# Kernel optimization log

Measured on AMD Instinct MI355X. Metric: run time of the kernel, lower is better.

Reference implementation:

```python
import jax, jax.numpy as jnp
import numpy as np

LOCAL_RANGE = 2
STRIDE = 2
NEG = 1e10

def stride_sparse_mask(N):
    i = np.arange(N)[:, None]
    j = np.arange(N)[None, :]
    d = np.abs(j - i)
    return ((d <= LOCAL_RANGE) | (d % STRIDE == 0)).astype(np.float32)

def setup_inputs() -> dict:
    key = jax.random.key(0)
    k1, k2, k3, k4 = jax.random.split(key, 4)
    B, S, D, H = 4, 2048, 512, 8
    # glorot-uniform-like scale for (D, D) weight slices
    lim = np.sqrt(6.0 / (D + D)).astype(np.float32)
    inputs = jax.random.normal(k1, (B, 1, S, D), dtype=jnp.float32)
    Wq = jax.random.uniform(k2, (H, D, D), minval=-lim, maxval=lim, dtype=jnp.float32)
    Wk = jax.random.uniform(k3, (H, D, D), minval=-lim, maxval=lim, dtype=jnp.float32)
    Wv = jax.random.uniform(k4, (H, D, D), minval=-lim, maxval=lim, dtype=jnp.float32)
    return {"inputs": inputs, "Wq": Wq, "Wk": Wk, "Wv": Wv}

def reference(inputs, Wq, Wk, Wv):
    # inputs: (B, 1, S, D); Wq/Wk/Wv: (H, D, D)
    B, _, S, D = inputs.shape
    H = Wq.shape[0]
    x = inputs[:, 0]  # (B, S, D)
    mask = jnp.asarray(stride_sparse_mask(S))  # (S, S), static
    # Batched over heads: equivalent to the original per-head Python loop.
    Q = jnp.einsum('bsd,hdk->bhsk', x, Wq)
    K = jnp.einsum('bsd,hdk->bhsk', x, Wk)
    V = jnp.einsum('bsd,hdk->bhsk', x, Wv)
    scores = jnp.einsum('bhsk,bhtk->bhst', Q, K) / jnp.sqrt(jnp.float32(D))
    # Original applies the 0/1 mask once (head 0) or twice (later heads);
    # double application is mathematically identical to a single one.
    scores = scores * mask - NEG * (1.0 - mask)
    attn = jax.nn.softmax(scores, axis=-1)
    out = jnp.einsum('bhst,bhtk->bhsk', attn, V)  # (B, H, S, D)
    total = jnp.mean(out, axis=1)  # average over heads
    return total[:, None, :, :]  # (B, 1, S, D)
```

## Files before the change

### kernel.cpp

```cpp
#include <hip/hip_runtime.h>
#include <stdint.h>

#define Bdim 4
#define Sdim 2048
#define Ddim 512
#define Hdim 8
#define Mdim (Bdim*Sdim)
#define Shalf 1024

typedef __attribute__((ext_vector_type(8))) short bf16x8;
typedef __attribute__((ext_vector_type(4))) float f32x4;
typedef __attribute__((ext_vector_type(4))) int i32x4;

#define SCALE 0.044194173824159216f
#define LOG2E 1.4426950408889634f

__device__ __forceinline__ unsigned short f2bf(float f){
  union { float f; unsigned int u; } v; v.f = f;
  unsigned int u = v.u + 0x7FFFu + ((v.u >> 16) & 1u);
  return (unsigned short)(u >> 16);
}

__device__ __forceinline__ void gl_lds16(const void* g, void* l){
  __builtin_amdgcn_global_load_lds(
      (const __attribute__((address_space(1))) unsigned int*)g,
      (__attribute__((address_space(3))) unsigned int*)l, 16, 0, 0);
}

__device__ __forceinline__ int permrow(int m){
  return (m & ~2047) | ((m & 1) << 10) | ((m & 2047) >> 1);
}

__global__ void cvt_x(const float* __restrict__ x, unsigned short* __restrict__ xb, int n8){
  int i = blockIdx.x*blockDim.x + threadIdx.x;
  if (i >= n8) return;
  const float4* p = (const float4*)x + (size_t)i*2;
  float4 a = p[0], b = p[1];
  union { unsigned short s[8]; i32x4 v; } o;
  o.s[0]=f2bf(a.x); o.s[1]=f2bf(a.y); o.s[2]=f2bf(a.z); o.s[3]=f2bf(a.w);
  o.s[4]=f2bf(b.x); o.s[5]=f2bf(b.y); o.s[6]=f2bf(b.z); o.s[7]=f2bf(b.w);
  ((i32x4*)xb)[i] = o.v;
}

__global__ void twk(const float* __restrict__ Wq, const float* __restrict__ Wk,
                    const float* __restrict__ Wv, unsigned short* __restrict__ Wt){
  __shared__ float t[32][33];
  int z = blockIdx.z;
  const float* W = (z < Hdim ? Wq : (z < 2*Hdim ? Wk : Wv)) + (size_t)(z % Hdim)*Ddim*Ddim;
  int n0 = blockIdx.x*32, k0 = blockIdx.y*32;
  #pragma unroll
  for (int i=0;i<4;i++){
    int k = k0 + threadIdx.y + i*8;
    t[threadIdx.y + i*8][threadIdx.x] = W[(size_t)k*Ddim + n0 + threadIdx.x];
  }
  __syncthreads();
  #pragma unroll
  for (int i=0;i<4;i++){
    int n = threadIdx.y + i*8;
    Wt[(size_t)z*Ddim*Ddim + (size_t)(n0+n)*Ddim + k0 + threadIdx.x] = f2bf(t[threadIdx.x][n]);
  }
}

__launch_bounds__(256, 2)
__global__ void proj(const unsigned short* __restrict__ xb,
                     const unsigned short* __restrict__ Wt,
                     unsigned short* __restrict__ Qb,
                     unsigned short* __restrict__ Kb,
                     unsigned short* __restrict__ Vtb,
                     int h0, int g)
{
  __shared__ unsigned short smem[16640];
  int tid = threadIdx.x, w = tid>>6, lane = tid&63;
  int wm = w>>1, wn = w&1;
  int y = blockIdx.y, g4 = 4*g;
  int type = y / g4; int rem = y - type*g4;
  int hrel = rem >> 2, nt = rem & 3;
  int m0 = blockIdx.x * 128, n0 = nt * 128;
  int l15 = lane&15, l4 = lane>>4;

  const unsigned short* Bsrc = Wt + (size_t)(type*Hdim + h0 + hrel)*Ddim*Ddim;

  f32x4 acc[4][4];
  #pragma unroll
  for (int i=0;i<4;i++)
    #pragma unroll
    for (int j=0;j<4;j++){ f32x4 z={0.f,0.f,0.f,0.f}; acc[i][j]=z; }

  for (int kt=0; kt<16; ++kt){
    int k0 = kt*32;
    #pragma unroll
    for (int i=0;i<2;i++){
      int row = i*64 + w*16 + (lane>>2);
      int cb  = lane&3;
      gl_lds16(xb   + (size_t)(m0+row)*Ddim + k0 + cb*8, (char*)smem + i*4096 + w*1024);
      gl_lds16(Bsrc + (size_t)(n0+row)*Ddim + k0 + cb*8, (char*)smem + 8192 + i*4096 + w*1024);
    }
    __syncthreads();
    bf16x8 af[4], bfr[4];
    #pragma unroll
    for (int i=0;i<4;i++){
      af[i]  = *(const bf16x8*)&smem[(wm*64 + i*16 + l15)*32 + l4*8];
      bfr[i] = *(const bf16x8*)&smem[4096 + (wn*64 + i*16 + l15)*32 + l4*8];
    }
    #pragma unroll
    for (int i=0;i<4;i++)
      #pragma unroll
      for (int j=0;j<4;j++)
        acc[i][j] = __builtin_amdgcn_mfma_f32_16x16x32_bf16(af[i], bfr[j], acc[i][j], 0,0,0);
    __syncthreads();
  }

  if (type < 2){
    unsigned short* Ob = (type==0 ? Qb : Kb) + (size_t)hrel*Mdim*Ddim;
    #pragma unroll
    for (int i=0;i<4;i++){
      int mb = m0 + wm*64 + i*16 + (l4<<2);
      #pragma unroll
      for (int j=0;j<4;j++){
        int col = n0 + wn*64 + j*16 + l15;
        #pragma unroll
        for (int r=0;r<4;r++)
          Ob[(size_t)permrow(mb + r)*Ddim + col] = f2bf(acc[i][j][r]);
      }
    }
  } else {
    #pragma unroll
    for (int i=0;i<4;i++){
      int ml = wm*64 + i*16 + (l4<<2);
      #pragma unroll
      for (int j=0;j<4;j++){
        int nl = wn*64 + j*16 + l15;
        #pragma unroll
        for (int r=0;r<4;r++)
          smem[(ml + r)*130 + nl] = f2bf(acc[i][j][r]);
      }
    }
    __syncthreads();
    unsigned short* Ovt = Vtb + (size_t)hrel*Ddim*Mdim;
    int bb  = m0 >> 11;
    int ib0 = (m0 & 2047) >> 1;
    #pragma unroll
    for (int c=0;c<8;c++){
      int nl = c*16 + (tid>>4);
      int il = (tid&15)*4;
      #pragma unroll
      for (int pp=0; pp<2; pp++){
        union { unsigned short s[4]; uint2 v; } pk;
        #pragma unroll
        for (int ii=0;ii<4;ii++) pk.s[ii] = smem[(2*(il+ii)+pp)*130 + nl];
        *(uint2*)&Ovt[(size_t)(n0+nl)*Mdim + bb*Sdim + pp*Shalf + ib0 + il] = pk.v;
      }
    }
  }
}

__device__ __forceinline__ void stage_dense(const unsigned short* Kbase, int krow0,
                                            const unsigned short* Vblk, int vcol0,
                                            char* KsB, char* VsB, int w, int lane)
{
  int l15 = lane&15, l4 = lane>>4;
  #pragma unroll
  for (int jj=0;jj<4;jj++){
    int bi = w*4 + jj;
    int row = krow0 + ((bi>>4)<<4) + l15;
    int g   = ((bi&15)<<2) + l4;
    gl_lds16(Kbase + ((size_t)row<<9) + g*8, KsB + bi*1024);
    int d   = (bi<<4) + l15;
    int col = vcol0 + l4*8;
    gl_lds16(Vblk + ((size_t)d<<13) + col, VsB + bi*1024);
  }
}
__device__ __forceinline__ void stage_spec(const unsigned short* Kbase, int krow0,
                                           const unsigned short* Vblk, int vcol0,
                                           char* KsB, char* VsB, int w, int lane)
{
  int l15 = lane&15, l4 = lane>>4;
  #pragma unroll
  for (int jj=0;jj<4;jj++){
    int bi = w*4 + jj;
    int row = krow0 + ((bi>>4)<<4) + l15;
    row = row < 0 ? 0 : (row > Shalf-1 ? Shalf-1 : row);
    int g   = ((bi&15)<<2) + l4;
    gl_lds16(Kbase + ((size_t)row<<9) + g*8, KsB + bi*1024);
    int d   = (bi<<4) + l15;
    int col = vcol0 + l4*8;
    col = col < 0 ? 0 : (col > Shalf-8 ? Shalf-8 : col);
    gl_lds16(Vblk + ((size_t)d<<13) + col, VsB + bi*1024);
  }
}

#define NDENSE 32
#define NSPEC 5
#define NT (NDENSE + NSPEC)

__launch_bounds__(512, 2)
__global__ void attn(const unsigned short* __restrict__ Qb,
                     const unsigned short* __restrict__ Kb,
                     const unsigned short* __restrict__ Vtb,
                     float* __restrict__ out)
{
  __shared__ char lds[2*32768 + 2*32768 + 8*1024];
  int tid = threadIdx.x, w = tid>>6, lane = tid&63;
  int l15 = lane&15, l4 = lane>>4;
  int z  = blockIdx.x;
  int qc = blockIdx.y;
  int p  = z & 1; int zb = z >> 1; int b = zb & 3; int h = zb >> 2;

  const unsigned short* Qp     = Qb + (size_t)h*Mdim*Ddim + (size_t)(b*Sdim + p*Shalf)*Ddim;
  const unsigned short* Ksame  = Kb + (size_t)h*Mdim*Ddim + (size_t)(b*Sdim + p*Shalf)*Ddim;
  const unsigned short* Kopp   = Kb + (size_t)h*Mdim*Ddim + (size_t)(b*Sdim + (1-p)*Shalf)*Ddim;
  const unsigned short* Vt     = Vtb + (size_t)h*Ddim*Mdim;
  int csame = b*Sdim + p*Shalf;
  int copp  = b*Sdim + (1-p)*Shalf;
  int i0 = qc*128;
  int j0 = i0 - 32 + 32*p;

  bf16x8 qa[16];
  {
    const unsigned short* qr = Qp + (size_t)(i0 + w*16 + l15)*Ddim;
    #pragma unroll
    for (int ks=0;ks<16;ks++) qa[ks] = *(const bf16x8*)&qr[ks*32 + l4*8];
  }

  f32x4 acc[32];
  #pragma unroll
  for (int n=0;n<32;n++){ f32x4 zz={0.f,0.f,0.f,0.f}; acc[n]=zz; }
  float ms[4], lp[4];
  #pragma unroll
  for (int r=0;r<4;r++){ ms[r] = -3.0e38f; lp[r] = 0.f; }

  stage_dense(Ksame, 0, Vt + csame, 0, lds, lds + 65536, w, lane);

  for (int t=0; t<NT; ++t){
    int buf = t & 1;
    char* KsB = lds + buf*32768;
    char* VsB = lds + 65536 + buf*32768;

    __builtin_amdgcn_sched_barrier(0);
    __builtin_amdgcn_s_barrier();
    if (t + 1 < NT){
      char* KsN = lds + (buf^1)*32768;
      char* VsN = lds + 65536 + (buf^1)*32768;
      if (t + 1 < NDENSE)
        stage_dense(Ksame, (t+1)*32, Vt + csame, (t+1)*32, KsN, VsN, w, lane);
      else {
        int tt = t + 1 - NDENSE;
        stage_spec(Kopp, j0 + tt*32, Vt + copp, j0 + tt*32, KsN, VsN, w, lane);
      }
      asm volatile("s_waitcnt vmcnt(8)" ::: "memory");
    } else {
      asm volatile("s_waitcnt vmcnt(0)" ::: "memory");
    }
    __builtin_amdgcn_s_barrier();
    __builtin_amdgcn_sched_barrier(0);

    f32x4 sc[2];
    #pragma unroll
    for (int sub=0; sub<2; ++sub){
      f32x4 ae = {0.f,0.f,0.f,0.f}, ao = {0.f,0.f,0.f,0.f};
      #pragma unroll
      for (int ks=0;ks<16;ks+=2){
        bf16x8 k0 = *(const bf16x8*)(KsB + (sub*16+ks)*1024   + (l4*16+l15)*16);
        bf16x8 k1 = *(const bf16x8*)(KsB + (sub*16+ks+1)*1024 + (l4*16+l15)*16);
        ae = __builtin_amdgcn_mfma_f32_16x16x32_bf16(qa[ks],   k0, ae, 0,0,0);
        ao = __builtin_amdgcn_mfma_f32_16x16x32_bf16(qa[ks+1], k1, ao, 0,0,0);
      }
      sc[sub] = ae + ao;
    }

    float s0v[4], s1v[4], lmax[4];
    bool spec = (t >= NDENSE);
    int tbase = spec ? (j0 + (t-NDENSE)*32) : 0;
    #pragma unroll
    for (int r=0;r<4;r++){
      float s0 = sc[0][r]*SCALE, s1 = sc[1][r]*SCALE;
      if (spec){
        int iq = i0 + w*16 + l4*4 + r;
        int jA = tbase + l15;
        int jB = jA + 16;
        int tgt = iq - 1 + 2*p;
        bool vA = (jA>=0) & (jA<Shalf) & ((jA==iq) | (jA==tgt));
        bool vB = (jB>=0) & (jB<Shalf) & ((jB==iq) | (jB==tgt));
        if(!vA) s0 = -1e30f;
        if(!vB) s1 = -1e30f;
      }
      s0v[r]=s0; s1v[r]=s1;
      lmax[r] = fmaxf(s0, s1);
    }
    bool need = (lmax[0] > ms[0]+8.f) | (lmax[1] > ms[1]+8.f) |
                (lmax[2] > ms[2]+8.f) | (lmax[3] > ms[3]+8.f);
    if (__any(need)){
      #pragma unroll
      for (int r=0;r<4;r++){
        float tm = lmax[r];
        tm = fmaxf(tm, __shfl_xor(tm, 1));
        tm = fmaxf(tm, __shfl_xor(tm, 2));
        tm = fmaxf(tm, __shfl_xor(tm, 4));
        tm = fmaxf(tm, __shfl_xor(tm, 8));
        float nm = fmaxf(ms[r], tm);
        float rs = exp2f((ms[r]-nm)*LOG2E);
        ms[r] = nm; lp[r] *= rs;
        #pragma unroll
        for (int n=0;n<32;n++) acc[n][r] *= rs;
      }
    }

    char* PsB = lds + 131072 + w*1024;
    #pragma unroll
    for (int r=0;r<4;r++){
      float p0 = exp2f((s0v[r]-ms[r])*LOG2E);
      float p1 = exp2f((s1v[r]-ms[r])*LOG2E);
      lp[r] += p0 + p1;
      int q = l4*4 + r;
      *(unsigned short*)(PsB + (((l15>>3)*16 + q)*16 + (l15&7)*2))     = f2bf(p0);
      *(unsigned short*)(PsB + (((2+(l15>>3))*16 + q)*16 + (l15&7)*2)) = f2bf(p1);
    }
    asm volatile("s_waitcnt lgkmcnt(0)" ::: "memory");
    __builtin_amdgcn_sched_barrier(0);
    bf16x8 pa = *(const bf16x8*)(PsB + (l4*16+l15)*16);

    #pragma unroll
    for (int n=0;n<32;n++){
      bf16x8 vb = *(const bf16x8*)(VsB + n*1024 + (l4*16+l15)*16);
      acc[n] = __builtin_amdgcn_mfma_f32_16x16x32_bf16(pa, vb, acc[n], 0,0,0);
    }
  }

  #pragma unroll
  for (int r=0;r<4;r++){
    float t = lp[r];
    t += __shfl_xor(t, 1);
    t += __shfl_xor(t, 2);
    t += __shfl_xor(t, 4);
    t += __shfl_xor(t, 8);
    float inv = 0.125f / t;
    int i = i0 + w*16 + l4*4 + r;
    float* orow = out + (size_t)(b*Sdim + 2*i + p)*Ddim;
    #pragma unroll
    for (int n=0;n<32;n++)
      atomicAdd(&orow[n*16 + l15], acc[n][r]*inv);
  }
}

extern "C" void kernel_launch(void* const* d_in, const int* in_sizes, int n_in,
                              void* d_out, int out_size, void* d_ws, size_t ws_size,
                              hipStream_t stream)
{
  (void)in_sizes; (void)n_in;
  const float* x  = (const float*)d_in[0];
  const float* Wq = (const float*)d_in[1];
  const float* Wk = (const float*)d_in[2];
  const float* Wv = (const float*)d_in[3];
  float* out = (float*)d_out;

  const size_t xb_bytes = (size_t)Mdim*Ddim*2;
  const size_t wt_bytes = (size_t)3*Hdim*Ddim*Ddim*2;
  const size_t per_head = (size_t)Mdim*Ddim*2;

  int g = 8;
  while (g > 1 && xb_bytes + wt_bytes + 3*(size_t)g*per_head > ws_size) g >>= 1;

  unsigned short* xb  = (unsigned short*)d_ws;
  unsigned short* Wt  = (unsigned short*)((char*)d_ws + xb_bytes);
  unsigned short* Qb  = (unsigned short*)((char*)d_ws + xb_bytes + wt_bytes);
  unsigned short* Kb  = Qb + (size_t)g*Mdim*Ddim;
  unsigned short* Vtb = Kb + (size_t)g*Mdim*Ddim;

  hipMemsetAsync(d_out, 0, (size_t)out_size*sizeof(float), stream);
  cvt_x<<<dim3(Mdim*Ddim/8/256), dim3(256), 0, stream>>>(x, xb, Mdim*Ddim/8);
  twk<<<dim3(Ddim/32, Ddim/32, 3*Hdim), dim3(32,8), 0, stream>>>(Wq, Wk, Wv, Wt);

  for (int h0 = 0; h0 < Hdim; h0 += g){
    proj<<<dim3(Mdim/128, 12*g), dim3(256), 0, stream>>>(xb, Wt, Qb, Kb, Vtb, h0, g);
    attn<<<dim3(g*Bdim*2, Shalf/128 ), dim3(512), 0, stream>>>(Qb, Kb, Vtb, out);
  }
}
```

Before: 586.8 us.

## Read V directly from global in attention and halve query tile per block

The attention kernel stops staging V tiles in LDS. Each wave now loads its V fragments straight from global memory inside the PV MFMA loop, and only K stays double-buffered in LDS. Blocks shrink to 4 waves covering 64 query rows, the grid doubles along the query axis, and the speculative opposite-parity tile count drops from 5 to 3 to match the smaller query span. This cuts LDS footprint and barrier-synchronised staging, but V is no longer shared through LDS, so each wave fetches it separately from L2 with more global traffic and exposed load latency in the PV loop.

```diff
diff --git a/kernel.cpp b/kernel.cpp
--- a/kernel.cpp
+++ b/kernel.cpp
@@ -154,52 +154,43 @@
   }
 }
 
-__device__ __forceinline__ void stage_dense(const unsigned short* Kbase, int krow0,
-                                            const unsigned short* Vblk, int vcol0,
-                                            char* KsB, char* VsB, int w, int lane)
+__device__ __forceinline__ void stage_k_dense(const unsigned short* Kbase, int krow0,
+                                              char* KsB, int w, int lane)
 {
   int l15 = lane&15, l4 = lane>>4;
   #pragma unroll
-  for (int jj=0;jj<4;jj++){
-    int bi = w*4 + jj;
+  for (int jj=0;jj<8;jj++){
+    int bi = w*8 + jj;
     int row = krow0 + ((bi>>4)<<4) + l15;
     int g   = ((bi&15)<<2) + l4;
     gl_lds16(Kbase + ((size_t)row<<9) + g*8, KsB + bi*1024);
-    int d   = (bi<<4) + l15;
-    int col = vcol0 + l4*8;
-    gl_lds16(Vblk + ((size_t)d<<13) + col, VsB + bi*1024);
-  }
-}
-__device__ __forceinline__ void stage_spec(const unsigned short* Kbase, int krow0,
-                                           const unsigned short* Vblk, int vcol0,
-                                           char* KsB, char* VsB, int w, int lane)
+  }
+}
+__device__ __forceinline__ void stage_k_spec(const unsigned short* Kbase, int krow0,
+                                             char* KsB, int w, int lane)
 {
   int l15 = lane&15, l4 = lane>>4;
   #pragma unroll
-  for (int jj=0;jj<4;jj++){
-    int bi = w*4 + jj;
+  for (int jj=0;jj<8;jj++){
+    int bi = w*8 + jj;
     int row = krow0 + ((bi>>4)<<4) + l15;
     row = row < 0 ? 0 : (row > Shalf-1 ? Shalf-1 : row);
     int g   = ((bi&15)<<2) + l4;
     gl_lds16(Kbase + ((size_t)row<<9) + g*8, KsB + bi*1024);
-    int d   = (bi<<4) + l15;
-    int col = vcol0 + l4*8;
-    col = col < 0 ? 0 : (col > Shalf-8 ? Shalf-8 : col);
-    gl_lds16(Vblk + ((size_t)d<<13) + col, VsB + bi*1024);
   }
 }
 
 #define NDENSE 32
-#define NSPEC 5
+#define NSPEC 3
 #define NT (NDENSE + NSPEC)
 
-__launch_bounds__(512, 2)
+__launch_bounds__(256, 2)
 __global__ void attn(const unsigned short* __restrict__ Qb,
                      const unsigned short* __restrict__ Kb,
                      const unsigned short* __restrict__ Vtb,
                      float* __restrict__ out)
 {
-  __shared__ char lds[2*32768 + 2*32768 + 8*1024];
+  __shared__ char lds[2*32768 + 4*1024];
   int tid = threadIdx.x, w = tid>>6, lane = tid&63;
   int l15 = lane&15, l4 = lane>>4;
   int z  = blockIdx.x;
@@ -212,7 +203,7 @@
   const unsigned short* Vt     = Vtb + (size_t)h*Ddim*Mdim;
   int csame = b*Sdim + p*Shalf;
   int copp  = b*Sdim + (1-p)*Shalf;
-  int i0 = qc*128;
+  int i0 = qc*64;
   int j0 = i0 - 32 + 32*p;
 
   bf16x8 qa[16];
@@ -229,24 +220,20 @@
   #pragma unroll
   for (int r=0;r<4;r++){ ms[r] = -3.0e38f; lp[r] = 0.f; }
 
-  stage_dense(Ksame, 0, Vt + csame, 0, lds, lds + 65536, w, lane);
+  stage_k_dense(Ksame, 0, lds, w, lane);
 
   for (int t=0; t<NT; ++t){
     int buf = t & 1;
     char* KsB = lds + buf*32768;
-    char* VsB = lds + 65536 + buf*32768;
 
     __builtin_amdgcn_sched_barrier(0);
     __builtin_amdgcn_s_barrier();
     if (t + 1 < NT){
       char* KsN = lds + (buf^1)*32768;
-      char* VsN = lds + 65536 + (buf^1)*32768;
       if (t + 1 < NDENSE)
-        stage_dense(Ksame, (t+1)*32, Vt + csame, (t+1)*32, KsN, VsN, w, lane);
-      else {
-        int tt = t + 1 - NDENSE;
-        stage_spec(Kopp, j0 + tt*32, Vt + copp, j0 + tt*32, KsN, VsN, w, lane);
-      }
+        stage_k_dense(Ksame, (t+1)*32, KsN, w, lane);
+      else
+        stage_k_spec(Kopp, j0 + (t+1-NDENSE)*32, KsN, w, lane);
       asm volatile("s_waitcnt vmcnt(8)" ::: "memory");
     } else {
       asm volatile("s_waitcnt vmcnt(0)" ::: "memory");
@@ -305,7 +292,7 @@
       }
     }
 
-    char* PsB = lds + 131072 + w*1024;
+    char* PsB = lds + 65536 + w*1024;
     #pragma unroll
     for (int r=0;r<4;r++){
       float p0 = exp2f((s0v[r]-ms[r])*LOG2E);
@@ -319,10 +306,20 @@
     __builtin_amdgcn_sched_barrier(0);
     bf16x8 pa = *(const bf16x8*)(PsB + (l4*16+l15)*16);
 
-    #pragma unroll
-    for (int n=0;n<32;n++){
-      bf16x8 vb = *(const bf16x8*)(VsB + n*1024 + (l4*16+l15)*16);
-      acc[n] = __builtin_amdgcn_mfma_f32_16x16x32_bf16(pa, vb, acc[n], 0,0,0);
+    {
+      int vcol;
+      if (!spec) vcol = csame + t*32 + l4*8;
+      else {
+        int rb = tbase + l4*8;
+        rb = rb < 0 ? 0 : (rb > Shalf-8 ? Shalf-8 : rb);
+        vcol = copp + rb;
+      }
+      const unsigned short* vptr = Vt + (size_t)l15*Mdim + vcol;
+      #pragma unroll
+      for (int n=0;n<32;n++){
+        bf16x8 vb = *(const bf16x8*)(vptr + (size_t)n*16*Mdim);
+        acc[n] = __builtin_amdgcn_mfma_f32_16x16x32_bf16(pa, vb, acc[n], 0,0,0);
+      }
     }
   }
 
@@ -372,6 +369,6 @@
 
   for (int h0 = 0; h0 < Hdim; h0 += g){
     proj<<<dim3(Mdim/128, 12*g), dim3(256), 0, stream>>>(xb, Wt, Qb, Kb, Vtb, h0, g);
-    attn<<<dim3(g*Bdim*2, Shalf/128 ), dim3(512), 0, stream>>>(Qb, Kb, Vtb, out);
-  }
-}
+    attn<<<dim3(g*Bdim*2, Shalf/64 ), dim3(256), 0, stream>>>(Qb, Kb, Vtb, out);
+  }
+}
```

New measurement: 1.023 ms. +74.3%, slower.

## Software-pipeline QK^T one tile ahead and split K/V staging loads

Applied to the files above, without the earlier changes.

Restructures the attention main loop so the QK^T scores for tile t+1 are computed before the softmax and PV of tile t. This gives the scheduler independent MFMA work to overlap with the softmax and exp latency. The K and V global-to-LDS loads are issued in two separate loops, K first, so a partial vmcnt wait of 4 releases the K half of the next tile while the V half is still in flight. The prologue preloads two tiles, and the next stage is issued after the PV step. This adds a register-resident sc_next array and more intricate barrier and waitcnt bookkeeping.

```diff
diff --git a/kernel.cpp b/kernel.cpp
--- a/kernel.cpp
+++ b/kernel.cpp
@@ -165,6 +165,10 @@
     int row = krow0 + ((bi>>4)<<4) + l15;
     int g   = ((bi&15)<<2) + l4;
     gl_lds16(Kbase + ((size_t)row<<9) + g*8, KsB + bi*1024);
+  }
+  #pragma unroll
+  for (int jj=0;jj<4;jj++){
+    int bi = w*4 + jj;
     int d   = (bi<<4) + l15;
     int col = vcol0 + l4*8;
     gl_lds16(Vblk + ((size_t)d<<13) + col, VsB + bi*1024);
@@ -182,6 +186,10 @@
     row = row < 0 ? 0 : (row > Shalf-1 ? Shalf-1 : row);
     int g   = ((bi&15)<<2) + l4;
     gl_lds16(Kbase + ((size_t)row<<9) + g*8, KsB + bi*1024);
+  }
+  #pragma unroll
+  for (int jj=0;jj<4;jj++){
+    int bi = w*4 + jj;
     int d   = (bi<<4) + l15;
     int col = vcol0 + l4*8;
     col = col < 0 ? 0 : (col > Shalf-8 ? Shalf-8 : col);
@@ -229,43 +237,40 @@
   #pragma unroll
   for (int r=0;r<4;r++){ ms[r] = -3.0e38f; lp[r] = 0.f; }
 
-  stage_dense(Ksame, 0, Vt + csame, 0, lds, lds + 65536, w, lane);
+  stage_dense(Ksame, 0,  Vt + csame, 0,  lds,         lds + 65536,         w, lane);
+  stage_dense(Ksame, 32, Vt + csame, 32, lds + 32768, lds + 65536 + 32768, w, lane);
+  asm volatile("s_waitcnt vmcnt(4)" ::: "memory");
+  __builtin_amdgcn_s_barrier();
+  __builtin_amdgcn_sched_barrier(0);
+
+  f32x4 sc_prev[2];
+  #pragma unroll
+  for (int sub=0; sub<2; ++sub){
+    f32x4 a0 = {0.f,0.f,0.f,0.f};
+    #pragma unroll
+    for (int ks=0;ks<16;ks++){
+      bf16x8 kb = *(const bf16x8*)(lds + (sub*16+ks)*1024 + (l4*16+l15)*16);
+      a0 = __builtin_amdgcn_mfma_f32_16x16x32_bf16(qa[ks], kb, a0, 0,0,0);
+    }
+    sc_prev[sub] = a0;
+  }
 
   for (int t=0; t<NT; ++t){
-    int buf = t & 1;
-    char* KsB = lds + buf*32768;
-    char* VsB = lds + 65536 + buf*32768;
-
-    __builtin_amdgcn_sched_barrier(0);
-    __builtin_amdgcn_s_barrier();
+    char* VsB = lds + 65536 + (t&1)*32768;
+
+    f32x4 sc_next[2];
     if (t + 1 < NT){
-      char* KsN = lds + (buf^1)*32768;
-      char* VsN = lds + 65536 + (buf^1)*32768;
-      if (t + 1 < NDENSE)
-        stage_dense(Ksame, (t+1)*32, Vt + csame, (t+1)*32, KsN, VsN, w, lane);
-      else {
-        int tt = t + 1 - NDENSE;
-        stage_spec(Kopp, j0 + tt*32, Vt + copp, j0 + tt*32, KsN, VsN, w, lane);
-      }
-      asm volatile("s_waitcnt vmcnt(8)" ::: "memory");
-    } else {
-      asm volatile("s_waitcnt vmcnt(0)" ::: "memory");
-    }
-    __builtin_amdgcn_s_barrier();
-    __builtin_amdgcn_sched_barrier(0);
-
-    f32x4 sc[2];
-    #pragma unroll
-    for (int sub=0; sub<2; ++sub){
-      f32x4 ae = {0.f,0.f,0.f,0.f}, ao = {0.f,0.f,0.f,0.f};
-      #pragma unroll
-      for (int ks=0;ks<16;ks+=2){
-        bf16x8 k0 = *(const bf16x8*)(KsB + (sub*16+ks)*1024   + (l4*16+l15)*16);
-        bf16x8 k1 = *(const bf16x8*)(KsB + (sub*16+ks+1)*1024 + (l4*16+l15)*16);
-        ae = __builtin_amdgcn_mfma_f32_16x16x32_bf16(qa[ks],   k0, ae, 0,0,0);
-        ao = __builtin_amdgcn_mfma_f32_16x16x32_bf16(qa[ks+1], k1, ao, 0,0,0);
-      }
-      sc[sub] = ae + ao;
+      char* KsN = lds + ((t+1)&1)*32768;
+      #pragma unroll
+      for (int sub=0; sub<2; ++sub){
+        f32x4 a0 = {0.f,0.f,0.f,0.f};
+        #pragma unroll
+        for (int ks=0;ks<16;ks++){
+          bf16x8 kb = *(const bf16x8*)(KsN + (sub*16+ks)*1024 + (l4*16+l15)*16);
+          a0 = __builtin_amdgcn_mfma_f32_16x16x32_bf16(qa[ks], kb, a0, 0,0,0);
+        }
+        sc_next[sub] = a0;
+      }
     }
 
     float s0v[4], s1v[4], lmax[4];
@@ -273,7 +278,7 @@
     int tbase = spec ? (j0 + (t-NDENSE)*32) : 0;
     #pragma unroll
     for (int r=0;r<4;r++){
-      float s0 = sc[0][r]*SCALE, s1 = sc[1][r]*SCALE;
+      float s0 = sc_prev[0][r]*SCALE, s1 = sc_prev[1][r]*SCALE;
       if (spec){
         int iq = i0 + w*16 + l4*4 + r;
         int jA = tbase + l15;
@@ -324,6 +329,30 @@
       bf16x8 vb = *(const bf16x8*)(VsB + n*1024 + (l4*16+l15)*16);
       acc[n] = __builtin_amdgcn_mfma_f32_16x16x32_bf16(pa, vb, acc[n], 0,0,0);
     }
+
+    __builtin_amdgcn_sched_barrier(0);
+    __builtin_amdgcn_s_barrier();
+    __builtin_amdgcn_sched_barrier(0);
+    if (t + 2 < NT){
+      int s = t + 2;
+      char* KsS = lds + (s&1)*32768;
+      char* VsS = lds + 65536 + (s&1)*32768;
+      if (s < NDENSE)
+        stage_dense(Ksame, s*32, Vt + csame, s*32, KsS, VsS, w, lane);
+      else
+        stage_spec(Kopp, j0 + (s-NDENSE)*32, Vt + copp, j0 + (s-NDENSE)*32, KsS, VsS, w, lane);
+    }
+    if (t + 1 < NT){
+      if (t + 2 < NT){
+        asm volatile("s_waitcnt vmcnt(4)" ::: "memory");
+      } else {
+        asm volatile("s_waitcnt vmcnt(0)" ::: "memory");
+      }
+      __builtin_amdgcn_s_barrier();
+      __builtin_amdgcn_sched_barrier(0);
+      sc_prev[0] = sc_next[0];
+      sc_prev[1] = sc_next[1];
+    }
   }
 
   #pragma unroll
```

After: 621.8 us. +6.0%, slower.

## Use 32x32 MFMA with wave-pair D split and drop online softmax max

Applied to the files above, without the earlier changes.

Reworks the attention loop to use 32x32x16 bf16 MFMAs. Each pair of waves splits the head dimension of QK^T and exchanges partial scores through LDS. The online max tracking and rescaling is replaced by a fixed exponent offset. The probability tile is packed in registers with cvt_pk_bf16 and permlane32_swap instead of being round-tripped through LDS. This trades an extra block barrier per tile and reliance on scores staying in exp range for fewer instructions and fewer shuffles.

```diff
diff --git a/kernel.cpp b/kernel.cpp
--- a/kernel.cpp
+++ b/kernel.cpp
@@ -10,6 +10,7 @@
 
 typedef __attribute__((ext_vector_type(8))) short bf16x8;
 typedef __attribute__((ext_vector_type(4))) float f32x4;
+typedef __attribute__((ext_vector_type(16))) float f32x16;
 typedef __attribute__((ext_vector_type(4))) int i32x4;
 
 #define SCALE 0.044194173824159216f
@@ -199,35 +200,43 @@
                      const unsigned short* __restrict__ Vtb,
                      float* __restrict__ out)
 {
-  __shared__ char lds[2*32768 + 2*32768 + 8*1024];
+  __shared__ char lds[163840];
   int tid = threadIdx.x, w = tid>>6, lane = tid&63;
-  int l15 = lane&15, l4 = lane>>4;
+  int qg = w>>1, dg = w&1;
+  int ql = lane&31, hh = lane>>5;
   int z  = blockIdx.x;
   int qc = blockIdx.y;
-  int p  = z & 1; int zb = z >> 1; int b = zb & 3; int h = zb >> 2;
-
-  const unsigned short* Qp     = Qb + (size_t)h*Mdim*Ddim + (size_t)(b*Sdim + p*Shalf)*Ddim;
-  const unsigned short* Ksame  = Kb + (size_t)h*Mdim*Ddim + (size_t)(b*Sdim + p*Shalf)*Ddim;
-  const unsigned short* Kopp   = Kb + (size_t)h*Mdim*Ddim + (size_t)(b*Sdim + (1-p)*Shalf)*Ddim;
-  const unsigned short* Vt     = Vtb + (size_t)h*Ddim*Mdim;
+  int p  = z & 1; int zb = z >> 1; int b = zb & 3; int hd = zb >> 2;
+
+  const unsigned short* Qp    = Qb + (size_t)hd*Mdim*Ddim + (size_t)(b*Sdim + p*Shalf)*Ddim;
+  const unsigned short* Ksame = Kb + (size_t)hd*Mdim*Ddim + (size_t)(b*Sdim + p*Shalf)*Ddim;
+  const unsigned short* Kopp  = Kb + (size_t)hd*Mdim*Ddim + (size_t)(b*Sdim + (1-p)*Shalf)*Ddim;
+  const unsigned short* Vt    = Vtb + (size_t)hd*Ddim*Mdim;
   int csame = b*Sdim + p*Shalf;
   int copp  = b*Sdim + (1-p)*Shalf;
   int i0 = qc*128;
   int j0 = i0 - 32 + 32*p;
 
-  bf16x8 qa[16];
+  const float C1 = SCALE*LOG2E;
+  const float C0 = -4.0f*LOG2E;
+
+  bf16x8 qf[16];
   {
-    const unsigned short* qr = Qp + (size_t)(i0 + w*16 + l15)*Ddim;
-    #pragma unroll
-    for (int ks=0;ks<16;ks++) qa[ks] = *(const bf16x8*)&qr[ks*32 + l4*8];
-  }
-
-  f32x4 acc[32];
-  #pragma unroll
-  for (int n=0;n<32;n++){ f32x4 zz={0.f,0.f,0.f,0.f}; acc[n]=zz; }
-  float ms[4], lp[4];
-  #pragma unroll
-  for (int r=0;r<4;r++){ ms[r] = -3.0e38f; lp[r] = 0.f; }
+    const unsigned short* qr = Qp + (size_t)(i0 + qg*32 + ql)*Ddim + dg*256 + hh*8;
+    #pragma unroll
+    for (int st=0; st<16; ++st) qf[st] = *(const bf16x8*)(qr + st*16);
+  }
+
+  f32x16 acc[8];
+  #pragma unroll
+  for (int dt=0; dt<8; ++dt)
+    #pragma unroll
+    for (int j=0; j<16; ++j) acc[dt][j] = 0.f;
+  float lp = 0.f;
+
+  char* Xch = lds + 131072;
+  int iq  = i0 + qg*32 + ql;
+  int tgt = iq - 1 + 2*p;
 
   stage_dense(Ksame, 0, Vt + csame, 0, lds, lds + 65536, w, lane);
 
@@ -254,91 +263,92 @@
     __builtin_amdgcn_s_barrier();
     __builtin_amdgcn_sched_barrier(0);
 
-    f32x4 sc[2];
-    #pragma unroll
-    for (int sub=0; sub<2; ++sub){
-      f32x4 ae = {0.f,0.f,0.f,0.f}, ao = {0.f,0.f,0.f,0.f};
-      #pragma unroll
-      for (int ks=0;ks<16;ks+=2){
-        bf16x8 k0 = *(const bf16x8*)(KsB + (sub*16+ks)*1024   + (l4*16+l15)*16);
-        bf16x8 k1 = *(const bf16x8*)(KsB + (sub*16+ks+1)*1024 + (l4*16+l15)*16);
-        ae = __builtin_amdgcn_mfma_f32_16x16x32_bf16(qa[ks],   k0, ae, 0,0,0);
-        ao = __builtin_amdgcn_mfma_f32_16x16x32_bf16(qa[ks+1], k1, ao, 0,0,0);
-      }
-      sc[sub] = ae + ao;
-    }
-
-    float s0v[4], s1v[4], lmax[4];
+    f32x16 sc;
+    #pragma unroll
+    for (int j=0; j<16; ++j) sc[j] = 0.f;
+    #pragma unroll
+    for (int st=0; st<16; ++st){
+      int c = dg*32 + st*2 + hh;
+      bf16x8 kf = *(const bf16x8*)(KsB + ((ql>>4)*16 + (c>>2))*1024 + (c&3)*256 + (ql&15)*16);
+      sc = __builtin_amdgcn_mfma_f32_32x32x16_bf16(kf, qf[st], sc, 0,0,0);
+    }
+
+    char* Xw = Xch + w*4096;
+    #pragma unroll
+    for (int i=0;i<4;i++){
+      f32x4 v;
+      #pragma unroll
+      for (int j=0;j<4;j++) v[j] = sc[4*i+j];
+      *(f32x4*)(Xw + i*1024 + lane*16) = v;
+    }
+    asm volatile("s_waitcnt lgkmcnt(0)" ::: "memory");
+    __builtin_amdgcn_sched_barrier(0);
+    __builtin_amdgcn_s_barrier();
+    __builtin_amdgcn_sched_barrier(0);
+
+    char* Xp = Xch + (w^1)*4096;
+    float pr[16];
     bool spec = (t >= NDENSE);
     int tbase = spec ? (j0 + (t-NDENSE)*32) : 0;
     #pragma unroll
-    for (int r=0;r<4;r++){
-      float s0 = sc[0][r]*SCALE, s1 = sc[1][r]*SCALE;
-      if (spec){
-        int iq = i0 + w*16 + l4*4 + r;
-        int jA = tbase + l15;
-        int jB = jA + 16;
-        int tgt = iq - 1 + 2*p;
-        bool vA = (jA>=0) & (jA<Shalf) & ((jA==iq) | (jA==tgt));
-        bool vB = (jB>=0) & (jB<Shalf) & ((jB==iq) | (jB==tgt));
-        if(!vA) s0 = -1e30f;
-        if(!vB) s1 = -1e30f;
-      }
-      s0v[r]=s0; s1v[r]=s1;
-      lmax[r] = fmaxf(s0, s1);
-    }
-    bool need = (lmax[0] > ms[0]+8.f) | (lmax[1] > ms[1]+8.f) |
-                (lmax[2] > ms[2]+8.f) | (lmax[3] > ms[3]+8.f);
-    if (__any(need)){
-      #pragma unroll
-      for (int r=0;r<4;r++){
-        float tm = lmax[r];
-        tm = fmaxf(tm, __shfl_xor(tm, 1));
-        tm = fmaxf(tm, __shfl_xor(tm, 2));
-        tm = fmaxf(tm, __shfl_xor(tm, 4));
-        tm = fmaxf(tm, __shfl_xor(tm, 8));
-        float nm = fmaxf(ms[r], tm);
-        float rs = exp2f((ms[r]-nm)*LOG2E);
-        ms[r] = nm; lp[r] *= rs;
-        #pragma unroll
-        for (int n=0;n<32;n++) acc[n][r] *= rs;
-      }
-    }
-
-    char* PsB = lds + 131072 + w*1024;
-    #pragma unroll
-    for (int r=0;r<4;r++){
-      float p0 = exp2f((s0v[r]-ms[r])*LOG2E);
-      float p1 = exp2f((s1v[r]-ms[r])*LOG2E);
-      lp[r] += p0 + p1;
-      int q = l4*4 + r;
-      *(unsigned short*)(PsB + (((l15>>3)*16 + q)*16 + (l15&7)*2))     = f2bf(p0);
-      *(unsigned short*)(PsB + (((2+(l15>>3))*16 + q)*16 + (l15&7)*2)) = f2bf(p1);
-    }
-    asm volatile("s_waitcnt lgkmcnt(0)" ::: "memory");
-    __builtin_amdgcn_sched_barrier(0);
-    bf16x8 pa = *(const bf16x8*)(PsB + (l4*16+l15)*16);
-
-    #pragma unroll
-    for (int n=0;n<32;n++){
-      bf16x8 vb = *(const bf16x8*)(VsB + n*1024 + (l4*16+l15)*16);
-      acc[n] = __builtin_amdgcn_mfma_f32_16x16x32_bf16(pa, vb, acc[n], 0,0,0);
-    }
-  }
-
-  #pragma unroll
-  for (int r=0;r<4;r++){
-    float t = lp[r];
-    t += __shfl_xor(t, 1);
-    t += __shfl_xor(t, 2);
-    t += __shfl_xor(t, 4);
-    t += __shfl_xor(t, 8);
-    float inv = 0.125f / t;
-    int i = i0 + w*16 + l4*4 + r;
-    float* orow = out + (size_t)(b*Sdim + 2*i + p)*Ddim;
-    #pragma unroll
-    for (int n=0;n<32;n++)
-      atomicAdd(&orow[n*16 + l15], acc[n][r]*inv);
+    for (int i=0;i<4;i++){
+      f32x4 v = *(const f32x4*)(Xp + i*1024 + lane*16);
+      #pragma unroll
+      for (int j=0;j<4;j++){
+        int r = 4*i+j;
+        float s = sc[r] + v[j];
+        float pe = exp2f(s*C1 + C0);
+        if (spec){
+          int jk = tbase + (r&3) + 8*(r>>2) + 4*hh;
+          bool ok = (jk>=0) & (jk<Shalf) & ((jk==iq) | (jk==tgt));
+          pe = ok ? pe : 0.f;
+        }
+        pr[r] = pe;
+        lp += pe;
+      }
+    }
+
+    union { unsigned int u[4]; bf16x8 v; } pa0, pa1;
+    {
+      unsigned int X, Y;
+      asm("v_cvt_pk_bf16_f32 %0, %1, %2" : "=v"(X) : "v"(pr[0]),  "v"(pr[1]));
+      asm("v_cvt_pk_bf16_f32 %0, %1, %2" : "=v"(Y) : "v"(pr[4]),  "v"(pr[5]));
+      asm("v_permlane32_swap_b32 %0, %1" : "+v"(X), "+v"(Y));
+      pa0.u[0] = X; pa0.u[2] = Y;
+      asm("v_cvt_pk_bf16_f32 %0, %1, %2" : "=v"(X) : "v"(pr[2]),  "v"(pr[3]));
+      asm("v_cvt_pk_bf16_f32 %0, %1, %2" : "=v"(Y) : "v"(pr[6]),  "v"(pr[7]));
+      asm("v_permlane32_swap_b32 %0, %1" : "+v"(X), "+v"(Y));
+      pa0.u[1] = X; pa0.u[3] = Y;
+      asm("v_cvt_pk_bf16_f32 %0, %1, %2" : "=v"(X) : "v"(pr[8]),  "v"(pr[9]));
+      asm("v_cvt_pk_bf16_f32 %0, %1, %2" : "=v"(Y) : "v"(pr[12]), "v"(pr[13]));
+      asm("v_permlane32_swap_b32 %0, %1" : "+v"(X), "+v"(Y));
+      pa1.u[0] = X; pa1.u[2] = Y;
+      asm("v_cvt_pk_bf16_f32 %0, %1, %2" : "=v"(X) : "v"(pr[10]), "v"(pr[11]));
+      asm("v_cvt_pk_bf16_f32 %0, %1, %2" : "=v"(Y) : "v"(pr[14]), "v"(pr[15]));
+      asm("v_permlane32_swap_b32 %0, %1" : "+v"(X), "+v"(Y));
+      pa1.u[1] = X; pa1.u[3] = Y;
+    }
+
+    #pragma unroll
+    for (int dt=0; dt<8; ++dt){
+      int bi = dg*16 + dt*2 + ((lane>>4)&1);
+      bf16x8 vf0 = *(const bf16x8*)(VsB + bi*1024 + hh*256 + (lane&15)*16);
+      acc[dt] = __builtin_amdgcn_mfma_f32_32x32x16_bf16(pa0.v, vf0, acc[dt], 0,0,0);
+      bf16x8 vf1 = *(const bf16x8*)(VsB + bi*1024 + (2+hh)*256 + (lane&15)*16);
+      acc[dt] = __builtin_amdgcn_mfma_f32_32x32x16_bf16(pa1.v, vf1, acc[dt], 0,0,0);
+    }
+  }
+
+  float lpq = lp + __shfl_xor(lp, 32);
+  #pragma unroll
+  for (int r=0;r<16;++r){
+    int qrow = (r&3) + 8*(r>>2) + 4*hh;
+    float inv = 0.125f / __shfl(lpq, qrow);
+    int orow = b*Sdim + 2*(i0 + qg*32 + qrow) + p;
+    float* op = out + (size_t)orow*Ddim + dg*256 + ql;
+    #pragma unroll
+    for (int dt=0; dt<8; ++dt)
+      atomicAdd(op + dt*32, acc[dt][r]*inv);
   }
 }
 
```

New measurement: 561.0 us. 4.4% less time.
